# Optimization experiments

Measured on AMD Instinct MI355X. Metric: run time of the kernel, lower is better.

Reference implementation:

```python
import jax, jax.numpy as jnp
import numpy as np

B, N, D, L, T = 64, 64, 128, 4, 10  # batch, atoms, hidden_dim, n_layers, n_atom_types
EPS = 1e-5


def setup_inputs() -> dict:
    key = jax.random.key(0)
    ks = jax.random.split(key, 10)
    def rn(k, shape, s=0.05):
        return jax.random.normal(k, shape, jnp.float32) * s
    return dict(
        positions=jax.random.normal(ks[0], (B, N, 3), jnp.float32),
        atomic_numbers=jax.random.randint(ks[1], (B, N), 0, T),
        embed=rn(ks[2], (T, D)),
        edge_w1=rn(ks[3], (L, 2 * D + 1, D)), edge_b1=jnp.zeros((L, D), jnp.float32),
        edge_w2=rn(ks[4], (L, D, D)), edge_b2=jnp.zeros((L, D), jnp.float32),
        node_w1=rn(ks[5], (L, 2 * D, D)), node_b1=jnp.zeros((L, D), jnp.float32),
        node_w2=rn(ks[6], (L, D, D)), node_b2=jnp.zeros((L, D), jnp.float32),
        ln_g=jnp.ones((L, D), jnp.float32), ln_b=jnp.zeros((L, D), jnp.float32),
        out_w=rn(ks[7], (D, 3)), out_b=jnp.zeros((3,), jnp.float32),
    )


def _layer(h, dist_sq, ew1, eb1, ew2, eb2, nw1, nb1, nw2, nb2, g, b):
    # edge_mlp first linear on cat([h_i, h_j, dist_sq]) == h@Wa (bcast over j)
    # + h@Wb (bcast over i) + dist_sq * w_d, avoiding materializing the concat.
    wa, wb, wd = ew1[:D], ew1[D:2 * D], ew1[2 * D]
    pre = (h @ wa)[:, :, None, :] + (h @ wb)[:, None, :, :] + dist_sq * wd + eb1  # [B,N,N,D]
    m_ij = jax.nn.silu(jax.nn.silu(pre) @ ew2 + eb2)
    m_i = m_ij.mean(axis=2)  # mean over j -> [B,N,D]
    # node_mlp on cat([h, m_i]) split the same way; dropout is eval-mode identity.
    h_out = jax.nn.silu(h @ nw1[:D] + m_i @ nw1[D:] + nb1) @ nw2 + nb2
    x = h + h_out
    mu = x.mean(-1, keepdims=True)
    var = ((x - mu) ** 2).mean(-1, keepdims=True)
    return (x - mu) / jnp.sqrt(var + EPS) * g + b


def reference(positions, atomic_numbers, embed, edge_w1, edge_b1, edge_w2, edge_b2,
              node_w1, node_b1, node_w2, node_b2, ln_g, ln_b, out_w, out_b):
    h = embed[atomic_numbers]  # [B,N,D]
    diff = positions[:, :, None, :] - positions[:, None, :, :]
    dist_sq = (diff ** 2).sum(-1, keepdims=True)  # [B,N,N,1]
    for i in range(L):
        h = _layer(h, dist_sq, edge_w1[i], edge_b1[i], edge_w2[i], edge_b2[i],
                   node_w1[i], node_b1[i], node_w2[i], node_b2[i], ln_g[i], ln_b[i])
    return h @ out_w + out_b  # [B,N,3]
```

## Files before the change

kernel.cpp:

```cpp
#include <hip/hip_runtime.h>
#include <hip/hip_fp16.h>


typedef _Float16 f16;
typedef _Float16 f16x8 __attribute__((ext_vector_type(8)));
typedef float f32x4 __attribute__((ext_vector_type(4)));

union H2x4 { f16x8 v; __half2 h[4]; };

__device__ __forceinline__ float bf2f(unsigned short u) {
    union { unsigned int i; float f; } v; v.i = ((unsigned int)u) << 16; return v.f;
}
__device__ __forceinline__ unsigned short f2bf(float f) {
    union { float f; unsigned int i; } v; v.f = f;
    unsigned int x = v.i;
    return (unsigned short)((x + 0x7fffu + ((x >> 16) & 1u)) >> 16);
}
__device__ __forceinline__ float silu_f(float x) {
    float e = __builtin_amdgcn_exp2f(-1.44269504088896f * x);
    return x * __builtin_amdgcn_rcpf(1.0f + e);
}
__device__ __forceinline__ __half2 silu_h2(__half2 x, __half2 kf, __half2 one2) {
    __half2 e = h2exp2(__hmul2(x, kf));
    return __hmul2(x, h2rcp(__hadd2(one2, e)));
}

struct Ptrs { const void* p[14]; };

__device__ __forceinline__ float ldf(const void* p, int i, int bf) {
    return bf ? bf2f(((const unsigned short*)p)[i]) : ((const float*)p)[i];
}

#define ELEM_TOTAL 393216
#define SMALL_TOTAL 17539

__global__ __launch_bounds__(256) void prep_kernel(
    Ptrs ptrs, f16* dst, float* sc)
{
    __shared__ int flgsh;
    int t = threadIdx.x;
    if (t < 64) {
        int ex = (((const unsigned short*)ptrs.p[0])[t * 2] >> 7) & 0xFF;
        unsigned long long m = __ballot(ex >= 110 && ex <= 135);
        if (t == 0) flgsh = (__popcll(m) >= 40) ? 1 : 0;
    }
    __syncthreads();
    int bf = flgsh;

    int gid = blockIdx.x * 256 + t;
    if (gid < ELEM_TOTAL) {
        int f = gid >> 3, j = gid & 7;
        int lay = f / 12288;
        int r   = f % 12288;
        const void* src; int base, rowoff = 0, r2;
        if (r < 6144) {
            int mat = r >> 11; r2 = r & 2047;
            if (mat == 0)      { src = ptrs.p[2]; base = lay * 32896; }
            else if (mat == 1) { src = ptrs.p[2]; base = lay * 32896; rowoff = 128; }
            else               { src = ptrs.p[4]; base = lay * 16384; }
        } else if (r < 10240) {
            r2 = r - 6144; src = ptrs.p[6]; base = lay * 32768;
        } else {
            r2 = r - 10240; src = ptrs.p[8]; base = lay * 16384;
        }
        int s = r2 >> 9, c = (r2 >> 6) & 7, l = r2 & 63;
        int row = rowoff + s * 32 + ((l >> 4) << 3) + j;
        int col = (c << 4) + (l & 15);
        dst[gid] = (f16)ldf(src, base + row * 128 + col, bf);
    } else {
        int sid = gid - ELEM_TOTAL;
        if (sid >= SMALL_TOTAL) return;
        const void* src; int i;
        if      (sid < 12288) { src = ptrs.p[0]; i = sid; }
        else if (sid < 13568) { src = ptrs.p[1]; i = sid - 12288; }
        else if (sid < 14080) { int k = sid - 13568;
                                src = ptrs.p[2]; i = (k >> 7) * 32896 + 32768 + (k & 127); }
        else if (sid < 14592) { src = ptrs.p[3];  i = sid - 14080; }
        else if (sid < 15104) { src = ptrs.p[5];  i = sid - 14592; }
        else if (sid < 15616) { src = ptrs.p[7];  i = sid - 15104; }
        else if (sid < 16128) { src = ptrs.p[9];  i = sid - 15616; }
        else if (sid < 16640) { src = ptrs.p[10]; i = sid - 16128; }
        else if (sid < 17152) { src = ptrs.p[11]; i = sid - 16640; }
        else if (sid < 17536) { src = ptrs.p[12]; i = sid - 17152; }
        else                  { src = ptrs.p[13]; i = sid - 17536; }
        sc[sid] = ldf(src, i, bf);
    }
}

__global__ __launch_bounds__(512) void embed_ab_kernel(
    const int* an, const float* sc, const f16* wa, const f16* wb,
    const float* eb1C, f16* h16, f16* a16, f16* b16)
{
    int t = threadIdx.x;
    int w = t >> 6, lane = t & 63;
    int row0 = blockIdx.x << 4;
    int m_ = lane & 15, q_ = lane >> 4;
    const float* emb = sc + 12288;
    int a = an[row0 + m_];
    a = a < 0 ? 0 : (a > 9 ? 9 : a);
    f16x8 afrag[4];
#pragma unroll
    for (int s = 0; s < 4; s++) {
        f32x4 u0 = *(const f32x4*)(emb + a * 128 + s * 32 + q_ * 8);
        f32x4 u1 = *(const f32x4*)(emb + a * 128 + s * 32 + q_ * 8 + 4);
        f16x8 hv;
#pragma unroll
        for (int e = 0; e < 4; e++) { hv[e] = (f16)u0[e]; hv[e + 4] = (f16)u1[e]; }
        afrag[s] = hv;
        if (w == 0)
            *(f16x8*)(h16 + (row0 + m_) * 128 + s * 32 + q_ * 8) = hv;
    }
    int c = w;
#pragma unroll
    for (int mat = 0; mat < 2; mat++) {
        const f16* W = mat ? wb : wa;
        f16* out     = mat ? b16 : a16;
        float init = mat ? 0.0f : eb1C[c * 16 + m_];
        f32x4 acc = { init, init, init, init };
#pragma unroll
        for (int s = 0; s < 4; s++) {
            f16x8 bfr = *(const f16x8*)(W + ((s * 8 + c) * 64 + lane) * 8);
            acc = __builtin_amdgcn_mfma_f32_16x16x32_f16(afrag[s], bfr, acc, 0, 0, 0);
        }
#pragma unroll
        for (int r = 0; r < 4; r++)
            out[(row0 + q_ * 4 + r) * 128 + c * 16 + m_] = (f16)acc[r];
    }
}

__global__ __launch_bounds__(512) void layer_kernel(
    const void* pos_raw, const float* sc, const f16* Wswz, int lay,
    f16* h16, f16* a16, const f16* bcur, f16* bnxt, void* out)
{
    __shared__ f16 S[2][64 * 136];
    __shared__ f16 b_lds[64 * 136];
    __shared__ f16 m_lds[16 * 136];
    __shared__ __half dsqh[1024];
    __shared__ __half2 wd2_sh[64];
    __shared__ float s1sh[8][16], s2sh[8][16];
    __shared__ float psh[8][16][3];
    __shared__ int flgsh;

    int t = threadIdx.x;
    int w = t >> 6, lane = t & 63;
    int m_ = lane & 15, q_ = lane >> 4;
    int c = w;
    int b  = blockIdx.x >> 2;
    int r0 = b * 64 + (blockIdx.x & 3) * 16;
    const int fin = (lay == 3);

    const f16* wl   = Wswz + lay * 98304;
    const f16* ew2s = wl + 32768;
    const f16* nw1s = wl + 49152;
    const f16* nw2s = wl + 81920;
    const float* posC = sc;
    const float* wdC  = sc + 13568 + lay * 128;
    const float* eb2C = sc + 14592 + lay * 128;
    const float* nb1C = sc + 15104 + lay * 128;
    const float* nb2C = sc + 15616 + lay * 128;
    const float* lngC = sc + 16128 + lay * 128;
    const float* lnbC = sc + 16640 + lay * 128;

    if (t < 64) {
        int ex = (((const unsigned short*)pos_raw)[t * 2] >> 7) & 0xFF;
        unsigned long long mk = __ballot(ex >= 110 && ex <= 135);
        if (t == 0) flgsh = (__popcll(mk) >= 40) ? 1 : 0;
    }

#pragma unroll
    for (int kk = 0; kk < 2; kk++) {
        int k = t + 512 * kk;
        int j = k >> 4, col0 = (k & 15) * 8;
        *(f16x8*)(b_lds + j * 136 + col0) =
            *(const f16x8*)(bcur + (b * 64 + j) * 128 + col0);
    }
#pragma unroll
    for (int kk = 0; kk < 2; kk++) {
        int k = t + 512 * kk;
        int i = k >> 6, j = k & 63;
        int gi = r0 + i, gj = b * 64 + j;
        float dx = posC[gi * 3 + 0] - posC[gj * 3 + 0];
        float dy = posC[gi * 3 + 1] - posC[gj * 3 + 1];
        float dz = posC[gi * 3 + 2] - posC[gj * 3 + 2];
        dsqh[k] = __float2half_rn(dx * dx + dy * dy + dz * dz);
    }
    if (t < 64) wd2_sh[t] = __floats2half2_rn(wdC[2 * t], wdC[2 * t + 1]);

    f16x8 bfr[4];
#pragma unroll
    for (int s = 0; s < 4; s++)
        bfr[s] = *(const f16x8*)(ew2s + ((s * 8 + c) * 64 + lane) * 8);
    float eb2v = eb2C[c * 16 + m_];
    const __half2 kf   = __floats2half2_rn(-1.44269504f, -1.44269504f);
    const __half2 one2 = __floats2half2_rn(1.0f, 1.0f);
    __syncthreads();

#define BUILD_S(I, SD)                                                        \
    {                                                                         \
        _Pragma("unroll")                                                     \
        for (int kk = 0; kk < 2; kk++) {                                      \
            int k = t + 512 * kk;                                             \
            int j = k >> 4, col0 = (k & 15) * 8;                              \
            __half dh = dsqh[(I) * 64 + j];                                   \
            __half2 ds2 = __halves2half2(dh, dh);                             \
            H2x4 av, bv, wv, sv;                                              \
            av.v = *(const f16x8*)(a16 + (r0 + (I)) * 128 + col0);            \
            bv.v = *(const f16x8*)(b_lds + j * 136 + col0);                   \
            wv.v = *(const f16x8*)((const f16*)wd2_sh + col0);                \
            _Pragma("unroll")                                                 \
            for (int e = 0; e < 4; e++) {                                     \
                __half2 pre = __hfma2(ds2, wv.h[e],                           \
                                      __hadd2(av.h[e], bv.h[e]));             \
                sv.h[e] = silu_h2(pre, kf, one2);                             \
            }                                                                 \
            *(f16x8*)((SD) + j * 136 + col0) = sv.v;                          \
        }                                                                     \
    }

    BUILD_S(0, S[0]);
    __syncthreads();

#pragma unroll 1
    for (int i = 0; i < 16; i++) {
        if (i < 15) BUILD_S(i + 1, S[(i + 1) & 1]);
        const f16* Sc = S[i & 1];
        f32x4 acc[4];
#pragma unroll
        for (int mb = 0; mb < 4; mb++)
            acc[mb] = (f32x4){ eb2v, eb2v, eb2v, eb2v };
#pragma unroll
        for (int s = 0; s < 4; s++)
#pragma unroll
            for (int mb = 0; mb < 4; mb++) {
                f16x8 af = *(const f16x8*)(Sc + (mb * 16 + m_) * 136 + s * 32 + q_ * 8);
                acc[mb] = __builtin_amdgcn_mfma_f32_16x16x32_f16(af, bfr[s], acc[mb], 0, 0, 0);
            }
        float red = 0.0f;
#pragma unroll
        for (int mb = 0; mb < 4; mb++)
#pragma unroll
            for (int r = 0; r < 4; r++)
                red += silu_f(acc[mb][r]);
        red += __shfl_xor(red, 16);
        red += __shfl_xor(red, 32);
        if (q_ == 0)
            m_lds[i * 136 + c * 16 + m_] = (f16)(red * 0.015625f);
        __syncthreads();
    }

    f16x8 af2[8];
#pragma unroll
    for (int s = 0; s < 4; s++) {
        af2[s]     = *(const f16x8*)(h16 + (r0 + m_) * 128 + s * 32 + q_ * 8);
        af2[s + 4] = *(const f16x8*)(m_lds + m_ * 136 + s * 32 + q_ * 8);
    }
    f16* relay = &S[0][0];
    {
        float e = nb1C[c * 16 + m_];
        f32x4 acc = { e, e, e, e };
#pragma unroll
        for (int s = 0; s < 8; s++) {
            f16x8 bv = *(const f16x8*)(nw1s + ((s * 8 + c) * 64 + lane) * 8);
            acc = __builtin_amdgcn_mfma_f32_16x16x32_f16(af2[s], bv, acc, 0, 0, 0);
        }
#pragma unroll
        for (int r = 0; r < 4; r++)
            relay[(q_ * 4 + r) * 136 + c * 16 + m_] = (f16)silu_f(acc[r]);
    }
    __syncthreads();
    f16x8 uf[4];
#pragma unroll
    for (int s = 0; s < 4; s++)
        uf[s] = *(const f16x8*)(relay + m_ * 136 + s * 32 + q_ * 8);
    float x[4];
    {
        float e = nb2C[c * 16 + m_];
        f32x4 acc = { e, e, e, e };
#pragma unroll
        for (int s = 0; s < 4; s++) {
            f16x8 bv = *(const f16x8*)(nw2s + ((s * 8 + c) * 64 + lane) * 8);
            acc = __builtin_amdgcn_mfma_f32_16x16x32_f16(uf[s], bv, acc, 0, 0, 0);
        }
#pragma unroll
        for (int r = 0; r < 4; r++)
            x[r] = acc[r] + (float)h16[(r0 + q_ * 4 + r) * 128 + c * 16 + m_];
    }
    float s1p[4], s2p[4];
#pragma unroll
    for (int r = 0; r < 4; r++) { s1p[r] = x[r]; s2p[r] = x[r] * x[r]; }
#pragma unroll
    for (int msk = 1; msk < 16; msk <<= 1)
#pragma unroll
        for (int r = 0; r < 4; r++) {
            s1p[r] += __shfl_xor(s1p[r], msk);
            s2p[r] += __shfl_xor(s2p[r], msk);
        }
    if (m_ == 0)
#pragma unroll
        for (int r = 0; r < 4; r++) {
            s1sh[w][q_ * 4 + r] = s1p[r];
            s2sh[w][q_ * 4 + r] = s2p[r];
        }
    __syncthreads();
    float mu[4], rs[4];
#pragma unroll
    for (int r = 0; r < 4; r++) {
        int row = q_ * 4 + r;
        float S1 = 0.f, S2 = 0.f;
#pragma unroll
        for (int w2 = 0; w2 < 8; w2++) { S1 += s1sh[w2][row]; S2 += s2sh[w2][row]; }
        mu[r] = S1 * (1.0f / 128.0f);
        float var = S2 * (1.0f / 128.0f) - mu[r] * mu[r];
        rs[r] = rsqrtf(var + 1e-5f);
    }

    if (!fin) {
#pragma unroll
        for (int r = 0; r < 4; r++) {
            int col = c * 16 + m_;
            int row = r0 + q_ * 4 + r;
            float y = (x[r] - mu[r]) * rs[r] * lngC[col] + lnbC[col];
            h16[row * 128 + col] = (f16)y;
            relay[(q_ * 4 + r) * 136 + col] = (f16)y;
        }
        __syncthreads();
        f16x8 hf[4];
#pragma unroll
        for (int s = 0; s < 4; s++)
            hf[s] = *(const f16x8*)(relay + m_ * 136 + s * 32 + q_ * 8);
        const f16* wlN = Wswz + (lay + 1) * 98304;
        const float* eb1N = sc + 14080 + (lay + 1) * 128;
#pragma unroll
        for (int mat = 0; mat < 2; mat++) {
            const f16* W = mat ? (wlN + 16384) : wlN;
            float init = mat ? 0.0f : eb1N[c * 16 + m_];
            f32x4 acc = { init, init, init, init };
#pragma unroll
            for (int s = 0; s < 4; s++) {
                f16x8 bv = *(const f16x8*)(W + ((s * 8 + c) * 64 + lane) * 8);
                acc = __builtin_amdgcn_mfma_f32_16x16x32_f16(hf[s], bv, acc, 0, 0, 0);
            }
#pragma unroll
            for (int r = 0; r < 4; r++) {
                if (mat == 0)
                    a16[(r0 + q_ * 4 + r) * 128 + c * 16 + m_] = (f16)acc[r];
                else
                    bnxt[(r0 + q_ * 4 + r) * 128 + c * 16 + m_] = (f16)acc[r];
            }
        }
    } else {
        const float* owC = sc + 17152;
        const float* obC = sc + 17536;
        float p[3][4];
#pragma unroll
        for (int r = 0; r < 4; r++) {
            int col = c * 16 + m_;
            float y = (x[r] - mu[r]) * rs[r] * lngC[col] + lnbC[col];
            p[0][r] = y * owC[col * 3 + 0];
            p[1][r] = y * owC[col * 3 + 1];
            p[2][r] = y * owC[col * 3 + 2];
        }
#pragma unroll
        for (int msk = 1; msk < 16; msk <<= 1)
#pragma unroll
            for (int k = 0; k < 3; k++)
#pragma unroll
                for (int r = 0; r < 4; r++)
                    p[k][r] += __shfl_xor(p[k][r], msk);
        if (m_ == 0)
#pragma unroll
            for (int r = 0; r < 4; r++)
#pragma unroll
                for (int k = 0; k < 3; k++)
                    psh[w][q_ * 4 + r][k] = p[k][r];
        __syncthreads();
        if (t < 16) {
            int row = r0 + t;
            int bf = flgsh;
#pragma unroll
            for (int k = 0; k < 3; k++) {
                float v = obC[k];
#pragma unroll
                for (int w2 = 0; w2 < 8; w2++) v += psh[w2][t][k];
                if (bf) ((unsigned short*)out)[row * 3 + k] = f2bf(v);
                else    ((float*)out)[row * 3 + k] = v;
            }
        }
    }
}

extern "C" void kernel_launch(void* const* d_in, const int* in_sizes, int n_in,
                              void* d_out, int out_size, void* d_ws, size_t ws_size,
                              hipStream_t stream)
{
    char* ws = (char*)d_ws;
    float* sc   = (float*)(ws + 1024);
    f16*   Wswz = (f16*)(ws + (128u << 10));
    f16*   h16  = (f16*)(ws + (1u << 20));
    f16*   a16  = (f16*)(ws + (2u << 20));
    f16*   b0   = (f16*)(ws + (3u << 20));
    f16*   b1   = (f16*)(ws + (4u << 20));

    Ptrs ptrs;
    const int src_idx[14] = {0, 2, 3, 4, 5, 6, 7, 8, 9, 10, 11, 12, 13, 14};
    for (int k = 0; k < 14; k++) ptrs.p[k] = d_in[src_idx[k]];

    prep_kernel<<<1605, 256, 0, stream>>>(ptrs, Wswz, sc);
    embed_ab_kernel<<<256, 512, 0, stream>>>((const int*)d_in[1], sc, Wswz,
                                             Wswz + 16384, sc + 14080,
                                             h16, a16, b0);
    for (int lay = 0; lay < 4; lay++) {
        const f16* bcur = (lay & 1) ? b1 : b0;
        f16*       bnxt = (lay & 1) ? b0 : b1;
        layer_kernel<<<256, 512, 0, stream>>>(d_in[0], sc, Wswz, lay,
                                              h16, a16, bcur, bnxt, d_out);
    }
}
```

Measured before the change: 209.0 us.

## Build edge activations in registers per wave and stage edge_w2 in LDS

Replaces the shared double-buffered S tile and its per-row block barriers with a scheme where each wave owns two source atoms i. The wave computes the silu(pre) fragments directly in registers in MFMA A-layout and loops over all eight output column blocks, reading the edge_w2 fragments from a full LDS copy. This removes the 16 __syncthreads in the edge loop and the LDS write/read round trip for S. In exchange every wave rereads edge_w2 from LDS for each column block, and the launch bound now requests higher occupancy, which may pressure registers.

Measured after the change: 475.8 us. 2.28x slower.

```diff
diff --git a/kernel.cpp b/kernel.cpp
--- a/kernel.cpp
+++ b/kernel.cpp
@@ -128,15 +128,16 @@
     }
 }
 
-__global__ __launch_bounds__(512) void layer_kernel(
+__global__ __launch_bounds__(512, 4) void layer_kernel(
     const void* pos_raw, const float* sc, const f16* Wswz, int lay,
     f16* h16, f16* a16, const f16* bcur, f16* bnxt, void* out)
 {
-    __shared__ f16 S[2][64 * 136];
+    __shared__ f16 ew2sl[16384];
     __shared__ f16 b_lds[64 * 136];
+    __shared__ f16 ar_lds[16 * 136];
     __shared__ f16 m_lds[16 * 136];
     __shared__ __half dsqh[1024];
-    __shared__ __half2 wd2_sh[64];
+    __shared__ f16 wd16[128];
     __shared__ float s1sh[8][16], s2sh[8][16];
     __shared__ float psh[8][16][3];
     __shared__ int flgsh;
@@ -168,11 +169,21 @@
     }
 
 #pragma unroll
+    for (int k = 0; k < 4; k++) {
+        int idx = (k * 512 + t) * 8;
+        *(f16x8*)(ew2sl + idx) = *(const f16x8*)(ew2s + idx);
+    }
+#pragma unroll
     for (int kk = 0; kk < 2; kk++) {
         int k = t + 512 * kk;
         int j = k >> 4, col0 = (k & 15) * 8;
         *(f16x8*)(b_lds + j * 136 + col0) =
             *(const f16x8*)(bcur + (b * 64 + j) * 128 + col0);
+    }
+    if (t < 256) {
+        int row = t >> 4, col0 = (t & 15) * 8;
+        *(f16x8*)(ar_lds + row * 136 + col0) =
+            *(const f16x8*)(a16 + (r0 + row) * 128 + col0);
     }
 #pragma unroll
     for (int kk = 0; kk < 2; kk++) {
@@ -184,69 +195,62 @@
         float dz = posC[gi * 3 + 2] - posC[gj * 3 + 2];
         dsqh[k] = __float2half_rn(dx * dx + dy * dy + dz * dz);
     }
-    if (t < 64) wd2_sh[t] = __floats2half2_rn(wdC[2 * t], wdC[2 * t + 1]);
-
-    f16x8 bfr[4];
-#pragma unroll
-    for (int s = 0; s < 4; s++)
-        bfr[s] = *(const f16x8*)(ew2s + ((s * 8 + c) * 64 + lane) * 8);
-    float eb2v = eb2C[c * 16 + m_];
-    const __half2 kf   = __floats2half2_rn(-1.44269504f, -1.44269504f);
-    const __half2 one2 = __floats2half2_rn(1.0f, 1.0f);
+    if (t < 128) wd16[t] = (f16)wdC[t];
     __syncthreads();
 
-#define BUILD_S(I, SD)                                                        \
-    {                                                                         \
-        _Pragma("unroll")                                                     \
-        for (int kk = 0; kk < 2; kk++) {                                      \
-            int k = t + 512 * kk;                                             \
-            int j = k >> 4, col0 = (k & 15) * 8;                              \
-            __half dh = dsqh[(I) * 64 + j];                                   \
-            __half2 ds2 = __halves2half2(dh, dh);                             \
-            H2x4 av, bv, wv, sv;                                              \
-            av.v = *(const f16x8*)(a16 + (r0 + (I)) * 128 + col0);            \
-            bv.v = *(const f16x8*)(b_lds + j * 136 + col0);                   \
-            wv.v = *(const f16x8*)((const f16*)wd2_sh + col0);                \
-            _Pragma("unroll")                                                 \
-            for (int e = 0; e < 4; e++) {                                     \
-                __half2 pre = __hfma2(ds2, wv.h[e],                           \
-                                      __hadd2(av.h[e], bv.h[e]));             \
-                sv.h[e] = silu_h2(pre, kf, one2);                             \
-            }                                                                 \
-            *(f16x8*)((SD) + j * 136 + col0) = sv.v;                          \
-        }                                                                     \
-    }
-
-    BUILD_S(0, S[0]);
+    {
+        float eb2v[8];
+#pragma unroll
+        for (int cc = 0; cc < 8; cc++) eb2v[cc] = eb2C[cc * 16 + m_];
+        const __half2 kf   = __floats2half2_rn(-1.44269504f, -1.44269504f);
+        const __half2 one2 = __floats2half2_rn(1.0f, 1.0f);
+#pragma unroll 1
+        for (int ii = 0; ii < 2; ii++) {
+            int i = w * 2 + ii;
+            float msum[8] = { 0.f, 0.f, 0.f, 0.f, 0.f, 0.f, 0.f, 0.f };
+#pragma unroll 1
+            for (int mb = 0; mb < 4; mb++) {
+                int j = mb * 16 + m_;
+                __half dh = dsqh[i * 64 + j];
+                __half2 ds2 = __halves2half2(dh, dh);
+                f16x8 sf[4];
+#pragma unroll
+                for (int s = 0; s < 4; s++) {
+                    H2x4 av, bv, wv, sv;
+                    av.v = *(const f16x8*)(ar_lds + i * 136 + s * 32 + q_ * 8);
+                    bv.v = *(const f16x8*)(b_lds + j * 136 + s * 32 + q_ * 8);
+                    wv.v = *(const f16x8*)(wd16 + s * 32 + q_ * 8);
+#pragma unroll
+                    for (int e = 0; e < 4; e++) {
+                        __half2 pre = __hfma2(ds2, wv.h[e],
+                                              __hadd2(av.h[e], bv.h[e]));
+                        sv.h[e] = silu_h2(pre, kf, one2);
+                    }
+                    sf[s] = sv.v;
+                }
+#pragma unroll
+                for (int cc = 0; cc < 8; cc++) {
+                    f32x4 acc = { eb2v[cc], eb2v[cc], eb2v[cc], eb2v[cc] };
+#pragma unroll
+                    for (int s = 0; s < 4; s++) {
+                        f16x8 wf = *(const f16x8*)(ew2sl + ((s * 8 + cc) * 64 + lane) * 8);
+                        acc = __builtin_amdgcn_mfma_f32_16x16x32_f16(sf[s], wf, acc, 0, 0, 0);
+                    }
+                    msum[cc] += silu_f(acc[0]) + silu_f(acc[1])
+                              + silu_f(acc[2]) + silu_f(acc[3]);
+                }
+            }
+#pragma unroll
+            for (int cc = 0; cc < 8; cc++) {
+                float red = msum[cc];
+                red += __shfl_xor(red, 16);
+                red += __shfl_xor(red, 32);
+                if (lane < 16)
+                    m_lds[i * 136 + cc * 16 + lane] = (f16)(red * 0.015625f);
+            }
+        }
+    }
     __syncthreads();
-
-#pragma unroll 1
-    for (int i = 0; i < 16; i++) {
-        if (i < 15) BUILD_S(i + 1, S[(i + 1) & 1]);
-        const f16* Sc = S[i & 1];
-        f32x4 acc[4];
-#pragma unroll
-        for (int mb = 0; mb < 4; mb++)
-            acc[mb] = (f32x4){ eb2v, eb2v, eb2v, eb2v };
-#pragma unroll
-        for (int s = 0; s < 4; s++)
-#pragma unroll
-            for (int mb = 0; mb < 4; mb++) {
-                f16x8 af = *(const f16x8*)(Sc + (mb * 16 + m_) * 136 + s * 32 + q_ * 8);
-                acc[mb] = __builtin_amdgcn_mfma_f32_16x16x32_f16(af, bfr[s], acc[mb], 0, 0, 0);
-            }
-        float red = 0.0f;
-#pragma unroll
-        for (int mb = 0; mb < 4; mb++)
-#pragma unroll
-            for (int r = 0; r < 4; r++)
-                red += silu_f(acc[mb][r]);
-        red += __shfl_xor(red, 16);
-        red += __shfl_xor(red, 32);
-        if (q_ == 0)
-            m_lds[i * 136 + c * 16 + m_] = (f16)(red * 0.015625f);
-        __syncthreads();
-    }
 
     f16x8 af2[8];
 #pragma unroll
@@ -254,7 +258,7 @@
         af2[s]     = *(const f16x8*)(h16 + (r0 + m_) * 128 + s * 32 + q_ * 8);
         af2[s + 4] = *(const f16x8*)(m_lds + m_ * 136 + s * 32 + q_ * 8);
     }
-    f16* relay = &S[0][0];
+    f16* relay = ar_lds;
     {
         float e = nb1C[c * 16 + m_];
         f32x4 acc = { e, e, e, e };
```
